# Performance work log

Measured on AMD Instinct MI355X. Metric: run time of the kernel, lower is better.

Reference implementation:

```python
import jax, jax.numpy as jnp
import numpy as np

N_NODES = 100000
N_EDGES = 1600000
D_FEAT = 64
ORDER = 2


def setup_inputs() -> dict:
    key = jax.random.key(0)
    k1, k2, k3, k4 = jax.random.split(key, 4)
    x = jax.random.normal(k1, (N_NODES, D_FEAT), dtype=jnp.float32)
    edge_row = jnp.sort(jax.random.randint(k2, (N_EDGES,), 0, N_NODES, dtype=jnp.int32))
    edge_col = jax.random.randint(k3, (N_EDGES,), 0, N_NODES, dtype=jnp.int32)
    # positive edge weights ~ normalized adjacency values
    edge_val = jax.random.uniform(k4, (N_EDGES,), dtype=jnp.float32)
    return {"x": x, "edge_row": edge_row, "edge_col": edge_col, "edge_val": edge_val}


def reference(x, edge_row, edge_col, edge_val):
    # SGConvolution: x <- adj @ x, repeated `order` times (no trainable params).
    # adj is sparse COO: adj[edge_row[e], edge_col[e]] = edge_val[e].
    def spmm(h):
        # gather source features, scale by edge weight, scatter-add to rows
        msg = edge_val[:, None] * h[edge_col]          # [E, D]
        return jax.ops.segment_sum(msg, edge_row, num_segments=N_NODES)  # [N, D]

    h = x
    for _ in range(ORDER):
        h = spmm(h)
    return h
```

## Files before the change

### kernel.cpp

```cpp
#include <hip/hip_runtime.h>
#include <hip/hip_fp16.h>


#define N_NODES 100000
#define N_EDGES 1600000
#define D_FEAT  64
#define ROWS    4

__device__ __forceinline__ float readlane_f(float x, int j) {
    return __uint_as_float(__builtin_amdgcn_readlane(__float_as_uint(x), j));
}

__device__ __forceinline__ void store_feat(__half* p, float v) { *p = __float2half_rn(v); }
__device__ __forceinline__ void store_feat(float*  p, float v) { *p = v; }

__global__ __launch_bounds__(256) void prep_kernel(
    const float* __restrict__ x, __half* __restrict__ h16,
    const int* __restrict__ erow, int* __restrict__ rowptr)
{
    const int gid = blockIdx.x * blockDim.x + threadIdx.x;
    const int n4  = (N_NODES * D_FEAT) / 4;
    if (gid < n4) {
        const float4 v = ((const float4*)x)[gid];
        ((__half2*)h16)[2 * gid]     = __floats2half2_rn(v.x, v.y);
        ((__half2*)h16)[2 * gid + 1] = __floats2half2_rn(v.z, v.w);
    } else {
        const int n = gid - n4;
        if (n <= N_NODES) {
            int lo = 0, hi = N_EDGES;
            while (lo < hi) {
                const int mid = (lo + hi) >> 1;
                if (erow[mid] < n) lo = mid + 1; else hi = mid;
            }
            rowptr[n] = lo;
        }
    }
}

template <typename OutT>
__global__ __launch_bounds__(256) void sg_spmm_csr(
    const __half* __restrict__ h,
    const int*    __restrict__ rowptr,
    const int*    __restrict__ ecol,
    const float*  __restrict__ eval,
    OutT*         __restrict__ out)
{
    const int lane = threadIdx.x & 63;
    const int wave = (int)((blockIdx.x * blockDim.x + threadIdx.x) >> 6);
    const int r0   = wave * ROWS;
    if (r0 >= N_NODES) return;

    int rp[ROWS + 1];
#pragma unroll
    for (int i = 0; i <= ROWS; ++i) rp[i] = rowptr[r0 + i];

    int c_v; float w_v;
    {
        const int e0 = rp[0], n = min(64, rp[1] - e0);
        c_v = (lane < n) ? ecol[e0 + lane] : 0;
        w_v = (lane < n) ? eval[e0 + lane] : 0.0f;
    }
    int nxt_c = 0; float nxt_w = 0.0f;

#pragma unroll
    for (int r = 0; r < ROWS; ++r) {
        if (r + 1 < ROWS) {
            const int e0 = rp[r + 1], n = min(64, rp[r + 2] - e0);
            nxt_c = (lane < n) ? ecol[e0 + lane] : 0;
            nxt_w = (lane < n) ? eval[e0 + lane] : 0.0f;
        }

        float acc = 0.0f;
        int eb = rp[r];
        const int e1 = rp[r + 1];
        while (eb < e1) {
            const int n   = min(64, e1 - eb);
            const int nch = (n + 15) >> 4;
            for (int k = 0; k < nch; ++k) {
                __half g[16];
#pragma unroll
                for (int j = 0; j < 16; ++j) {
                    const int c = __builtin_amdgcn_readlane(c_v, k * 16 + j);
                    g[j] = h[(size_t)c * D_FEAT + lane];
                }
#pragma unroll
                for (int j = 0; j < 16; ++j) {
                    acc += readlane_f(w_v, k * 16 + j) * __half2float(g[j]);
                }
            }
            eb += 64;
            if (eb < e1) {
                const int n2 = min(64, e1 - eb);
                c_v = (lane < n2) ? ecol[eb + lane] : 0;
                w_v = (lane < n2) ? eval[eb + lane] : 0.0f;
            }
        }
        store_feat(&out[(size_t)(r0 + r) * D_FEAT + lane], acc);
        if (r + 1 < ROWS) { c_v = nxt_c; w_v = nxt_w; }
    }
}

__global__ __launch_bounds__(256) void spmm_atomic_f32(
    const float* __restrict__ h, const int* __restrict__ erow,
    const int* __restrict__ ecol, const float* __restrict__ eval,
    float* __restrict__ out)
{
    const int lane  = threadIdx.x & 63;
    const int wave  = (int)((blockIdx.x * blockDim.x + threadIdx.x) >> 6);
    const int start = wave * 64;
    if (start >= N_EDGES) return;
    int cur_row = erow[start];
    float acc = 0.0f;
    for (int e = start; e < start + 64; ++e) {
        const int r = erow[e];
        if (r != cur_row) {
            atomicAdd(&out[(size_t)cur_row * D_FEAT + lane], acc);
            acc = 0.0f; cur_row = r;
        }
        acc += eval[e] * h[(size_t)ecol[e] * D_FEAT + lane];
    }
    atomicAdd(&out[(size_t)cur_row * D_FEAT + lane], acc);
}

extern "C" void kernel_launch(void* const* d_in, const int* in_sizes, int n_in,
                              void* d_out, int out_size, void* d_ws, size_t ws_size,
                              hipStream_t stream) {
    const float* x    = (const float*)d_in[0];
    const int*   erow = (const int*)  d_in[1];
    const int*   ecol = (const int*)  d_in[2];
    const float* eval = (const float*)d_in[3];
    float*       out  = (float*)d_out;

    const size_t n_elem    = (size_t)N_NODES * D_FEAT;
    const size_t f16_bytes = n_elem * sizeof(__half);
    const size_t off_a     = 1 << 20;
    const size_t off_b     = off_a + f16_bytes;
    const size_t needed    = off_b + f16_bytes;

    const int threads = 256;

    if (ws_size >= needed) {
        int*    rowptr = (int*)d_ws;
        __half* h16a   = (__half*)((char*)d_ws + off_a);
        __half* h16b   = (__half*)((char*)d_ws + off_b);

        const int prep_total  = (int)(n_elem / 4) + N_NODES + 1;
        const int prep_blocks = (prep_total + threads - 1) / threads;
        const int spmm_blocks = (N_NODES / ROWS) * 64 / threads;

        prep_kernel<<<prep_blocks, threads, 0, stream>>>(x, h16a, erow, rowptr);
        sg_spmm_csr<__half><<<spmm_blocks, threads, 0, stream>>>(
            h16a, rowptr, ecol, eval, h16b);
        sg_spmm_csr<float><<<spmm_blocks, threads, 0, stream>>>(
            h16b, rowptr, ecol, eval, out);
    } else {
        float* h1 = (float*)d_ws;
        const size_t f32_bytes = n_elem * sizeof(float);
        hipMemsetAsync(h1, 0, f32_bytes, stream);
        hipMemsetAsync(out, 0, f32_bytes, stream);
        const int blocks = (N_EDGES / 64) * 64 / threads;
        spmm_atomic_f32<<<blocks, threads, 0, stream>>>(x, erow, ecol, eval, h1);
        spmm_atomic_f32<<<blocks, threads, 0, stream>>>(h1, erow, ecol, eval, out);
    }
}
```

Before: 171.4 us.

## Process wave's rows as one merged edge stream with double-buffered gathers

Instead of looping over each of the four rows separately, the kernel walks the contiguous edge range of all four rows in 64-edge chunks, flushing the accumulator when an edge crosses a row boundary. Gathers for the next 16-edge group are issued before the current group is accumulated, using a two-slot register buffer to overlap memory latency with FMAs. This removes per-row partial chunks and short-row underutilization, at the cost of a per-edge boundary check inside the inner loop and extra register pressure.

```diff
diff --git a/kernel.cpp b/kernel.cpp
--- a/kernel.cpp
+++ b/kernel.cpp
@@ -50,53 +50,55 @@
     const int r0   = wave * ROWS;
     if (r0 >= N_NODES) return;
 
-    int rp[ROWS + 1];
+    const int rp0 = __builtin_amdgcn_readfirstlane(rowptr[r0 + 0]);
+    const int rp1 = __builtin_amdgcn_readfirstlane(rowptr[r0 + 1]);
+    const int rp2 = __builtin_amdgcn_readfirstlane(rowptr[r0 + 2]);
+    const int rp3 = __builtin_amdgcn_readfirstlane(rowptr[r0 + 3]);
+    const int rp4 = __builtin_amdgcn_readfirstlane(rowptr[r0 + 4]);
+
+    float acc = 0.0f;
+    int   r   = 0;
+    int   bnd = rp1;
+
+    for (int eb = rp0; eb < rp4; eb += 64) {
+        const int n = min(64, rp4 - eb);
+        const int   c_v = (lane < n) ? ecol[eb + lane] : 0;
+        const float w_v = (lane < n) ? eval[eb + lane] : 0.0f;
+
+        __half g[2][16];
 #pragma unroll
-    for (int i = 0; i <= ROWS; ++i) rp[i] = rowptr[r0 + i];
-
-    int c_v; float w_v;
-    {
-        const int e0 = rp[0], n = min(64, rp[1] - e0);
-        c_v = (lane < n) ? ecol[e0 + lane] : 0;
-        w_v = (lane < n) ? eval[e0 + lane] : 0.0f;
-    }
-    int nxt_c = 0; float nxt_w = 0.0f;
-
+        for (int j = 0; j < 16; ++j) {
+            const int c = __builtin_amdgcn_readlane(c_v, j);
+            g[0][j] = h[(size_t)c * D_FEAT + lane];
+        }
 #pragma unroll
-    for (int r = 0; r < ROWS; ++r) {
-        if (r + 1 < ROWS) {
-            const int e0 = rp[r + 1], n = min(64, rp[r + 2] - e0);
-            nxt_c = (lane < n) ? ecol[e0 + lane] : 0;
-            nxt_w = (lane < n) ? eval[e0 + lane] : 0.0f;
-        }
-
-        float acc = 0.0f;
-        int eb = rp[r];
-        const int e1 = rp[r + 1];
-        while (eb < e1) {
-            const int n   = min(64, e1 - eb);
-            const int nch = (n + 15) >> 4;
-            for (int k = 0; k < nch; ++k) {
-                __half g[16];
+        for (int k = 0; k < 4; ++k) {
+            if (k * 16 < n) {
+                if ((k + 1) * 16 < n) {
 #pragma unroll
-                for (int j = 0; j < 16; ++j) {
-                    const int c = __builtin_amdgcn_readlane(c_v, k * 16 + j);
-                    g[j] = h[(size_t)c * D_FEAT + lane];
+                    for (int j = 0; j < 16; ++j) {
+                        const int c = __builtin_amdgcn_readlane(c_v, (k + 1) * 16 + j);
+                        g[(k + 1) & 1][j] = h[(size_t)c * D_FEAT + lane];
+                    }
                 }
 #pragma unroll
                 for (int j = 0; j < 16; ++j) {
-                    acc += readlane_f(w_v, k * 16 + j) * __half2float(g[j]);
+                    const int e = eb + k * 16 + j;
+                    while (r < ROWS && e >= bnd) {
+                        store_feat(&out[(size_t)(r0 + r) * D_FEAT + lane], acc);
+                        acc = 0.0f;
+                        ++r;
+                        bnd = (r == 1) ? rp2 : (r == 2) ? rp3 : rp4;
+                    }
+                    acc += readlane_f(w_v, k * 16 + j) * __half2float(g[k & 1][j]);
                 }
             }
-            eb += 64;
-            if (eb < e1) {
-                const int n2 = min(64, e1 - eb);
-                c_v = (lane < n2) ? ecol[eb + lane] : 0;
-                w_v = (lane < n2) ? eval[eb + lane] : 0.0f;
-            }
         }
+    }
+    while (r < ROWS) {
         store_feat(&out[(size_t)(r0 + r) * D_FEAT + lane], acc);
-        if (r + 1 < ROWS) { c_v = nxt_c; w_v = nxt_w; }
+        acc = 0.0f;
+        ++r;
     }
 }
 
```

Result: no change. 173.3 us (+1.1%).
